# Optimization experiments

Hardware: AMD Instinct MI355X
Metric: run time of the kernel (lower is better)

Reference implementation:

```python
import jax, jax.numpy as jnp
import numpy as np

B, H, S, D = 2, 16, 1024, 64  # batch, n_heads, seq_len, d_k
NEG = -1.0e9


def setup_inputs() -> dict:
    key = jax.random.key(0)
    kq, kk, kv, kt, kf, km, kd = jax.random.split(key, 7)
    Q = jax.random.normal(kq, (B, H, S, D), dtype=jnp.float32)
    K = jax.random.normal(kk, (B, H, S, D), dtype=jnp.float32)
    V = jax.random.normal(kv, (B, H, S, D), dtype=jnp.float32)
    ia_type = jax.random.normal(kt, (B, H, S, S), dtype=jnp.float32)
    ia_feat = jax.random.normal(kf, (B, H, S, S), dtype=jnp.float32)
    attn_mask_if = jax.random.bernoulli(km, 0.1, (B, H, S, S))
    attn_mask = attn_mask_if  # passed to forward but unused, as in the source
    distance_matrix = jax.random.normal(kd, (B, S, S), dtype=jnp.float32)
    return {"Q": Q, "K": K, "V": V, "attn_mask": attn_mask,
            "attn_mask_if": attn_mask_if, "ia_type": ia_type,
            "ia_feat": ia_feat, "distance_matrix": distance_matrix}


def reference(Q, K, V, attn_mask, attn_mask_if, ia_type, ia_feat, distance_matrix):
    # scores1 = Q K^T / sqrt(d_k)
    scores1 = jnp.einsum("bhqd,bhkd->bhqk", Q, K) / jnp.sqrt(jnp.float32(D))
    # bias masked to -1e9, then scores masked again to -1e9 => masked entries are exactly -1e9
    scores = jnp.where(attn_mask_if, NEG, scores1 + ia_type + ia_feat)
    attn = jax.nn.softmax(scores, axis=-1)
    context = jnp.einsum("bhqk,bhkd->bhqd", attn, V)
    return context, attn
```

## Files before the change

### kernel.cpp

```cpp
#include <hip/hip_runtime.h>
#include <math.h>

#define S_LEN 1024
#define D_DIM 64
#define NEGV  (-1.0e9f)
#define PSTR  1040

__global__ __launch_bounds__(256, 1)
void attn_bias_fused(const float* __restrict__ Q, const float* __restrict__ K,
                     const float* __restrict__ V, const int* __restrict__ mif,
                     const float* __restrict__ iat, const float* __restrict__ iaf,
                     float* __restrict__ ctx, float* __restrict__ attn)
{
    __shared__ float  Qst[D_DIM][16];
    __shared__ float4 Kt4[D_DIM][64];
    __shared__ float  P[16][PSTR];

    const int tid  = threadIdx.x;
    const int wave = tid >> 6;
    const int lane = tid & 63;
    const int bh   = blockIdx.x >> 6;
    const int qb   = (blockIdx.x & 63) << 4;

    const float* Qb = Q + ((size_t)(bh * S_LEN + qb)) * D_DIM;
    const float* Kb = K + ((size_t)bh * S_LEN) * D_DIM;
    const float* Vb = V + ((size_t)bh * S_LEN) * D_DIM;

    {
        int q = tid >> 4;
        int l = tid & 15;
        float4 v = *(const float4*)(Qb + (size_t)q * D_DIM + l * 4);
        Qst[4 * l + 0][q] = v.x;
        Qst[4 * l + 1][q] = v.y;
        Qst[4 * l + 2][q] = v.z;
        Qst[4 * l + 3][q] = v.w;
    }

    const int kg = lane;
    const int qg = wave;

    for (int c = 0; c < 4; ++c) {
        __syncthreads();
        {
            int l   = tid & 15;
            int kr0 = tid >> 4;
            #pragma unroll
            for (int i = 0; i < 16; ++i) {
                int kk = i * 16 + kr0;
                float4 v = *(const float4*)(Kb + (size_t)(c * 256 + kk) * D_DIM + l * 4);
                int cc  = (kk >> 2) ^ (l & 7);
                int sub = kk & 3;
                ((float*)&Kt4[4 * l + 0][cc])[sub] = v.x;
                ((float*)&Kt4[4 * l + 1][cc])[sub] = v.y;
                ((float*)&Kt4[4 * l + 2][cc])[sub] = v.z;
                ((float*)&Kt4[4 * l + 3][cc])[sub] = v.w;
            }
        }
        __syncthreads();

        float4 bt[4], bf[4];
        int4   bm[4];
        #pragma unroll
        for (int i = 0; i < 4; ++i) {
            size_t off = ((size_t)(bh * S_LEN + qb + qg * 4 + i)) * S_LEN + c * 256 + kg * 4;
            bt[i] = *(const float4*)(iat + off);
            bf[i] = *(const float4*)(iaf + off);
            bm[i] = *(const int4*)(mif + off);
        }

        float4 a0 = {0.f, 0.f, 0.f, 0.f}, a1 = a0, a2 = a0, a3 = a0;
        #pragma unroll 16
        for (int d = 0; d < D_DIM; ++d) {
            float4 kv = Kt4[d][kg ^ ((d >> 2) & 7)];
            float4 qv = *(const float4*)&Qst[d][qg * 4];
            a0.x = fmaf(qv.x, kv.x, a0.x); a0.y = fmaf(qv.x, kv.y, a0.y);
            a0.z = fmaf(qv.x, kv.z, a0.z); a0.w = fmaf(qv.x, kv.w, a0.w);
            a1.x = fmaf(qv.y, kv.x, a1.x); a1.y = fmaf(qv.y, kv.y, a1.y);
            a1.z = fmaf(qv.y, kv.z, a1.z); a1.w = fmaf(qv.y, kv.w, a1.w);
            a2.x = fmaf(qv.z, kv.x, a2.x); a2.y = fmaf(qv.z, kv.y, a2.y);
            a2.z = fmaf(qv.z, kv.z, a2.z); a2.w = fmaf(qv.z, kv.w, a2.w);
            a3.x = fmaf(qv.w, kv.x, a3.x); a3.y = fmaf(qv.w, kv.y, a3.y);
            a3.z = fmaf(qv.w, kv.z, a3.z); a3.w = fmaf(qv.w, kv.w, a3.w);
        }

        float4 av[4] = {a0, a1, a2, a3};
        #pragma unroll
        for (int i = 0; i < 4; ++i) {
            float4 s = av[i];
            float4 t = bt[i], f = bf[i];
            int4   m = bm[i];
            s.x = m.x ? NEGV : fmaf(s.x, 0.125f, t.x + f.x);
            s.y = m.y ? NEGV : fmaf(s.y, 0.125f, t.y + f.y);
            s.z = m.z ? NEGV : fmaf(s.z, 0.125f, t.z + f.z);
            s.w = m.w ? NEGV : fmaf(s.w, 0.125f, t.w + f.w);
            *(float4*)&P[qg * 4 + i][c * 256 + kg * 4] = s;
        }
    }
    __syncthreads();

    {
        int r  = wave * 4 + (lane >> 4);
        int ks = lane & 15;
        float* Prow = P[r];
        float mx = -INFINITY;
        #pragma unroll
        for (int j = 0; j < 16; ++j) {
            float4 v = *(const float4*)&Prow[(ks + 16 * j) * 4];
            mx = fmaxf(mx, fmaxf(fmaxf(v.x, v.y), fmaxf(v.z, v.w)));
        }
        #pragma unroll
        for (int s = 1; s < 16; s <<= 1) mx = fmaxf(mx, __shfl_xor(mx, s, 64));

        float sum = 0.f;
        #pragma unroll
        for (int j = 0; j < 16; ++j) {
            float4 v = *(const float4*)&Prow[(ks + 16 * j) * 4];
            v.x = __expf(v.x - mx);
            v.y = __expf(v.y - mx);
            v.z = __expf(v.z - mx);
            v.w = __expf(v.w - mx);
            sum += v.x + v.y + v.z + v.w;
            *(float4*)&Prow[(ks + 16 * j) * 4] = v;
        }
        #pragma unroll
        for (int s = 1; s < 16; s <<= 1) sum += __shfl_xor(sum, s, 64);
        float rinv = 1.f / sum;

        float* arow = attn + ((size_t)(bh * S_LEN + qb + r)) * S_LEN;
        #pragma unroll
        for (int j = 0; j < 16; ++j) {
            float4 v = *(const float4*)&Prow[(ks + 16 * j) * 4];
            v.x *= rinv; v.y *= rinv; v.z *= rinv; v.w *= rinv;
            *(float4*)&Prow[(ks + 16 * j) * 4] = v;
            *(float4*)(arow + (ks + 16 * j) * 4) = v;
        }
    }
    __syncthreads();

    {
        int dg = lane & 15;
        int ks = lane >> 4;
        float4 accv[16];
        #pragma unroll
        for (int q = 0; q < 16; ++q) accv[q] = make_float4(0.f, 0.f, 0.f, 0.f);

        #pragma unroll 2
        for (int i = 0; i < 16; ++i) {
            int k0 = wave * 256 + i * 16 + ks * 4;
            const float* vrow = Vb + (size_t)k0 * D_DIM + dg * 4;
            float4 v0 = *(const float4*)(vrow + 0 * D_DIM);
            float4 v1 = *(const float4*)(vrow + 1 * D_DIM);
            float4 v2 = *(const float4*)(vrow + 2 * D_DIM);
            float4 v3 = *(const float4*)(vrow + 3 * D_DIM);
            #pragma unroll
            for (int q = 0; q < 16; ++q) {
                float4 p = *(const float4*)&P[q][k0];
                float4 a = accv[q];
                a.x = fmaf(p.x, v0.x, a.x); a.x = fmaf(p.y, v1.x, a.x);
                a.x = fmaf(p.z, v2.x, a.x); a.x = fmaf(p.w, v3.x, a.x);
                a.y = fmaf(p.x, v0.y, a.y); a.y = fmaf(p.y, v1.y, a.y);
                a.y = fmaf(p.z, v2.y, a.y); a.y = fmaf(p.w, v3.y, a.y);
                a.z = fmaf(p.x, v0.z, a.z); a.z = fmaf(p.y, v1.z, a.z);
                a.z = fmaf(p.z, v2.z, a.z); a.z = fmaf(p.w, v3.z, a.z);
                a.w = fmaf(p.x, v0.w, a.w); a.w = fmaf(p.y, v1.w, a.w);
                a.w = fmaf(p.z, v2.w, a.w); a.w = fmaf(p.w, v3.w, a.w);
                accv[q] = a;
            }
        }

        float* part = (float*)Kt4;
        int base = (wave * 4 + ks) * 1024 + dg * 4;
        #pragma unroll
        for (int q = 0; q < 16; ++q)
            *(float4*)(part + base + q * 64) = accv[q];
        __syncthreads();

        int q  = tid >> 4;
        int dr = tid & 15;
        float4 r = make_float4(0.f, 0.f, 0.f, 0.f);
        #pragma unroll
        for (int s = 0; s < 16; ++s) {
            float4 v = *(const float4*)(part + s * 1024 + q * 64 + dr * 4);
            r.x += v.x; r.y += v.y; r.z += v.z; r.w += v.w;
        }
        *(float4*)(ctx + ((size_t)(bh * S_LEN + qb + q)) * D_DIM + dr * 4) = r;
    }
}

extern "C" void kernel_launch(void* const* d_in, const int* in_sizes, int n_in,
                              void* d_out, int out_size, void* d_ws, size_t ws_size,
                              hipStream_t stream) {
    const float* Q   = (const float*)d_in[0];
    const float* K   = (const float*)d_in[1];
    const float* V   = (const float*)d_in[2];
    const int*   mif = (const int*)d_in[4];
    const float* iat = (const float*)d_in[5];
    const float* iaf = (const float*)d_in[6];

    float* ctx  = (float*)d_out;
    float* attn = (float*)d_out + (size_t)2 * 16 * 1024 * 64;

    dim3 grid(2048), block(256);
    hipLaunchKernelGGL(attn_bias_fused, grid, block, 0, stream,
                       Q, K, V, mif, iat, iaf, ctx, attn);
}
```

Baseline: 631.3 us.

## Keep scores in registers, alias P onto K buffer, and shrink LDS for two blocks

Scores are now kept in registers (sc[16]) across the four key chunks, and softmax runs directly on them with full-wave shuffles instead of a separate 65KB P array in shared memory. The normalized probabilities are written into the reused Kt4 buffer. The cross-wave context reduction uses shuffles plus a small scratch area aliased with Qst. Together these cut LDS usage enough to allow launch_bounds(256,2), i.e. two blocks per CU, at the cost of more register pressure and extra barriers.

```diff
diff --git a/kernel.cpp b/kernel.cpp
--- a/kernel.cpp
+++ b/kernel.cpp
@@ -4,17 +4,18 @@
 #define S_LEN 1024
 #define D_DIM 64
 #define NEGV  (-1.0e9f)
-#define PSTR  1040
-
-__global__ __launch_bounds__(256, 1)
+
+__global__ __launch_bounds__(256, 2)
 void attn_bias_fused(const float* __restrict__ Q, const float* __restrict__ K,
                      const float* __restrict__ V, const int* __restrict__ mif,
                      const float* __restrict__ iat, const float* __restrict__ iaf,
                      float* __restrict__ ctx, float* __restrict__ attn)
 {
-    __shared__ float  Qst[D_DIM][16];
     __shared__ float4 Kt4[D_DIM][64];
-    __shared__ float  P[16][PSTR];
+    __shared__ float  SB[2048];
+
+    float* Pn = (float*)Kt4;
+    float (*Qst)[16] = (float(*)[16])SB;
 
     const int tid  = threadIdx.x;
     const int wave = tid >> 6;
@@ -27,8 +28,7 @@
     const float* Vb = V + ((size_t)bh * S_LEN) * D_DIM;
 
     {
-        int q = tid >> 4;
-        int l = tid & 15;
+        int q = tid >> 4, l = tid & 15;
         float4 v = *(const float4*)(Qb + (size_t)q * D_DIM + l * 4);
         Qst[4 * l + 0][q] = v.x;
         Qst[4 * l + 1][q] = v.y;
@@ -39,11 +39,13 @@
     const int kg = lane;
     const int qg = wave;
 
+    float4 sc[16];
+
+    #pragma unroll
     for (int c = 0; c < 4; ++c) {
         __syncthreads();
         {
-            int l   = tid & 15;
-            int kr0 = tid >> 4;
+            int l = tid & 15, kr0 = tid >> 4;
             #pragma unroll
             for (int i = 0; i < 16; ++i) {
                 int kk = i * 16 + kr0;
@@ -93,56 +95,65 @@
             s.y = m.y ? NEGV : fmaf(s.y, 0.125f, t.y + f.y);
             s.z = m.z ? NEGV : fmaf(s.z, 0.125f, t.z + f.z);
             s.w = m.w ? NEGV : fmaf(s.w, 0.125f, t.w + f.w);
-            *(float4*)&P[qg * 4 + i][c * 256 + kg * 4] = s;
+            sc[c * 4 + i] = s;
         }
     }
     __syncthreads();
 
     {
-        int r  = wave * 4 + (lane >> 4);
-        int ks = lane & 15;
-        float* Prow = P[r];
-        float mx = -INFINITY;
-        #pragma unroll
-        for (int j = 0; j < 16; ++j) {
-            float4 v = *(const float4*)&Prow[(ks + 16 * j) * 4];
-            mx = fmaxf(mx, fmaxf(fmaxf(v.x, v.y), fmaxf(v.z, v.w)));
-        }
-        #pragma unroll
-        for (int s = 1; s < 16; s <<= 1) mx = fmaxf(mx, __shfl_xor(mx, s, 64));
-
-        float sum = 0.f;
-        #pragma unroll
-        for (int j = 0; j < 16; ++j) {
-            float4 v = *(const float4*)&Prow[(ks + 16 * j) * 4];
-            v.x = __expf(v.x - mx);
-            v.y = __expf(v.y - mx);
-            v.z = __expf(v.z - mx);
-            v.w = __expf(v.w - mx);
-            sum += v.x + v.y + v.z + v.w;
-            *(float4*)&Prow[(ks + 16 * j) * 4] = v;
-        }
-        #pragma unroll
-        for (int s = 1; s < 16; s <<= 1) sum += __shfl_xor(sum, s, 64);
-        float rinv = 1.f / sum;
-
-        float* arow = attn + ((size_t)(bh * S_LEN + qb + r)) * S_LEN;
-        #pragma unroll
-        for (int j = 0; j < 16; ++j) {
-            float4 v = *(const float4*)&Prow[(ks + 16 * j) * 4];
-            v.x *= rinv; v.y *= rinv; v.z *= rinv; v.w *= rinv;
-            *(float4*)&Prow[(ks + 16 * j) * 4] = v;
-            *(float4*)(arow + (ks + 16 * j) * 4) = v;
-        }
+        float mx[4], sum[4], rinv[4];
+        #pragma unroll
+        for (int i = 0; i < 4; ++i) {
+            float m = -INFINITY;
+            #pragma unroll
+            for (int c = 0; c < 4; ++c) {
+                float4 v = sc[c * 4 + i];
+                m = fmaxf(m, fmaxf(fmaxf(v.x, v.y), fmaxf(v.z, v.w)));
+            }
+            #pragma unroll
+            for (int s = 1; s < 64; s <<= 1) m = fmaxf(m, __shfl_xor(m, s, 64));
+            mx[i] = m;
+        }
+        #pragma unroll
+        for (int i = 0; i < 4; ++i) {
+            float sm = 0.f;
+            #pragma unroll
+            for (int c = 0; c < 4; ++c) {
+                float4 v = sc[c * 4 + i];
+                v.x = __expf(v.x - mx[i]);
+                v.y = __expf(v.y - mx[i]);
+                v.z = __expf(v.z - mx[i]);
+                v.w = __expf(v.w - mx[i]);
+                sc[c * 4 + i] = v;
+                sm += v.x + v.y + v.z + v.w;
+            }
+            #pragma unroll
+            for (int s = 1; s < 64; s <<= 1) sm += __shfl_xor(sm, s, 64);
+            sum[i] = sm;
+            rinv[i] = 1.f / sm;
+        }
+        #pragma unroll
+        for (int i = 0; i < 4; ++i) {
+            int r = qg * 4 + i;
+            float* arow = attn + ((size_t)(bh * S_LEN + qb + r)) * S_LEN;
+            #pragma unroll
+            for (int c = 0; c < 4; ++c) {
+                float4 v = sc[c * 4 + i];
+                v.x *= rinv[i]; v.y *= rinv[i]; v.z *= rinv[i]; v.w *= rinv[i];
+                *(float4*)(arow + c * 256 + kg * 4)  = v;
+                *(float4*)&Pn[r * 1024 + c * 256 + kg * 4] = v;
+            }
+        }
+        (void)sum;
     }
     __syncthreads();
 
     {
         int dg = lane & 15;
         int ks = lane >> 4;
-        float4 accv[16];
-        #pragma unroll
-        for (int q = 0; q < 16; ++q) accv[q] = make_float4(0.f, 0.f, 0.f, 0.f);
+        float4 acc[16];
+        #pragma unroll
+        for (int q = 0; q < 16; ++q) acc[q] = make_float4(0.f, 0.f, 0.f, 0.f);
 
         #pragma unroll 2
         for (int i = 0; i < 16; ++i) {
@@ -154,8 +165,8 @@
             float4 v3 = *(const float4*)(vrow + 3 * D_DIM);
             #pragma unroll
             for (int q = 0; q < 16; ++q) {
-                float4 p = *(const float4*)&P[q][k0];
-                float4 a = accv[q];
+                float4 p = *(const float4*)&Pn[q * 1024 + k0];
+                float4 a = acc[q];
                 a.x = fmaf(p.x, v0.x, a.x); a.x = fmaf(p.y, v1.x, a.x);
                 a.x = fmaf(p.z, v2.x, a.x); a.x = fmaf(p.w, v3.x, a.x);
                 a.y = fmaf(p.x, v0.y, a.y); a.y = fmaf(p.y, v1.y, a.y);
@@ -164,26 +175,44 @@
                 a.z = fmaf(p.z, v2.z, a.z); a.z = fmaf(p.w, v3.z, a.z);
                 a.w = fmaf(p.x, v0.w, a.w); a.w = fmaf(p.y, v1.w, a.w);
                 a.w = fmaf(p.z, v2.w, a.w); a.w = fmaf(p.w, v3.w, a.w);
-                accv[q] = a;
-            }
-        }
-
-        float* part = (float*)Kt4;
-        int base = (wave * 4 + ks) * 1024 + dg * 4;
-        #pragma unroll
-        for (int q = 0; q < 16; ++q)
-            *(float4*)(part + base + q * 64) = accv[q];
-        __syncthreads();
-
-        int q  = tid >> 4;
-        int dr = tid & 15;
-        float4 r = make_float4(0.f, 0.f, 0.f, 0.f);
-        #pragma unroll
-        for (int s = 0; s < 16; ++s) {
-            float4 v = *(const float4*)(part + s * 1024 + q * 64 + dr * 4);
-            r.x += v.x; r.y += v.y; r.z += v.z; r.w += v.w;
-        }
-        *(float4*)(ctx + ((size_t)(bh * S_LEN + qb + q)) * D_DIM + dr * 4) = r;
+                acc[q] = a;
+            }
+        }
+
+        #pragma unroll
+        for (int q = 0; q < 16; ++q) {
+            acc[q].x += __shfl_xor(acc[q].x, 16, 64);
+            acc[q].y += __shfl_xor(acc[q].y, 16, 64);
+            acc[q].z += __shfl_xor(acc[q].z, 16, 64);
+            acc[q].w += __shfl_xor(acc[q].w, 16, 64);
+            acc[q].x += __shfl_xor(acc[q].x, 32, 64);
+            acc[q].y += __shfl_xor(acc[q].y, 32, 64);
+            acc[q].z += __shfl_xor(acc[q].z, 32, 64);
+            acc[q].w += __shfl_xor(acc[q].w, 32, 64);
+        }
+
+        float* scratch = SB;
+        #pragma unroll
+        for (int qh = 0; qh < 2; ++qh) {
+            __syncthreads();
+            if (lane < 16) {
+                #pragma unroll
+                for (int j = 0; j < 8; ++j)
+                    *(float4*)&scratch[(wave * 8 + j) * 64 + dg * 4] = acc[qh * 8 + j];
+            }
+            __syncthreads();
+            if (tid < 128) {
+                int qq = tid >> 4;
+                int dr = tid & 15;
+                float4 r = make_float4(0.f, 0.f, 0.f, 0.f);
+                #pragma unroll
+                for (int s = 0; s < 4; ++s) {
+                    float4 v = *(const float4*)&scratch[(s * 8 + qq) * 64 + dr * 4];
+                    r.x += v.x; r.y += v.y; r.z += v.z; r.w += v.w;
+                }
+                *(float4*)(ctx + ((size_t)(bh * S_LEN + qb + qh * 8 + qq)) * D_DIM + dr * 4) = r;
+            }
+        }
     }
 }
 
```

New measurement: 538.9 us. 14.6% less time.
